# Optimization experiments

Hardware: AMD Instinct MI355X
Metric: run time of the kernel (lower is better)

The kernel has to match this reference:

```python
import jax, jax.numpy as jnp
import numpy as np

N_NODES = 100000
N_EDGES = 600000
HIDDEN = 128
BN_EPS = 1e-5


def setup_inputs() -> dict:
    key = jax.random.key(0)
    k_x, k_e, k_w, k_b, k_g = jax.random.split(key, 5)
    x = jax.random.normal(k_x, (N_NODES, HIDDEN), dtype=jnp.float32)
    edge_index = jax.random.randint(k_e, (2, N_EDGES), 0, N_NODES, dtype=jnp.int64)
    # GCNConv linear weight (no bias on the linear; bias added post-aggregation)
    scale = 1.0 / np.sqrt(HIDDEN)
    W = jax.random.uniform(k_w, (HIDDEN, HIDDEN), jnp.float32, -scale, scale)
    b = jax.random.uniform(k_b, (HIDDEN,), jnp.float32, -scale, scale)
    gamma = jnp.ones((HIDDEN,), jnp.float32)   # BatchNorm weight
    beta = jnp.zeros((HIDDEN,), jnp.float32)   # BatchNorm bias
    return {"x": x, "edge_index": edge_index, "W": W, "b": b, "gamma": gamma, "beta": beta}


def reference(x, edge_index, W, b, gamma, beta):
    N = x.shape[0]
    # ReLU then GCNConv linear transform: [N, D]
    h = jnp.matmul(jax.nn.relu(x), W)
    # Add self-loops (PyG GCNConv default)
    loops = jnp.arange(N, dtype=edge_index.dtype)
    row = jnp.concatenate([edge_index[0], loops])  # source nodes
    col = jnp.concatenate([edge_index[1], loops])  # target nodes
    # Symmetric normalization deg^{-1/2} with unit edge weights
    ones = jnp.ones(row.shape[0], dtype=h.dtype)
    deg = jax.ops.segment_sum(ones, col, num_segments=N)
    dinv = jnp.where(deg > 0, jax.lax.rsqrt(deg), 0.0)
    norm = dinv[row] * dinv[col]  # [E+N]
    # Gather -> scale -> scatter-add aggregation, then conv bias
    agg = jax.ops.segment_sum(norm[:, None] * h[row], col, num_segments=N)
    out = agg + b
    # BatchNorm1d (training mode: batch stats, biased variance)
    mean = jnp.mean(out, axis=0)
    var = jnp.var(out, axis=0)
    return gamma * (out - mean) * jax.lax.rsqrt(var + BN_EPS) + beta
```

## Files before the change

kernel.cpp:

```cpp
#include <hip/hip_runtime.h>

#define D 128
#define CAP 32
#define BN_EPS 1e-5f

typedef float floatx4 __attribute__((ext_vector_type(4)));
typedef __bf16 bf16x8 __attribute__((ext_vector_type(8)));

__device__ inline unsigned short f2bf(float f) {
    unsigned u; __builtin_memcpy(&u, &f, 4);
    unsigned r = (u + 0x7FFFu + ((u >> 16) & 1u)) >> 16;
    return (unsigned short)r;
}
__device__ inline float bflo(unsigned v) { unsigned x = v << 16; float f; __builtin_memcpy(&f, &x, 4); return f; }
__device__ inline float bfhi(unsigned v) { unsigned x = v & 0xFFFF0000u; float f; __builtin_memcpy(&f, &x, 4); return f; }

__global__ void setup_k(const unsigned* __restrict__ e, int* __restrict__ flag,
                        int* __restrict__ cursor, float* __restrict__ sums,
                        float* __restrict__ sumsq, const float* __restrict__ W,
                        unsigned short* __restrict__ Wt, int n_nodes) {
    int i = blockIdx.x * blockDim.x + threadIdx.x;
    if (i < n_nodes) cursor[i] = 0;
    if (i < D) { sums[i] = 0.f; sumsq[i] = 0.f; }
    if (i < D * D) {
        int n = i >> 7, k = i & 127;
        Wt[n * D + k] = f2bf(W[k * D + n]);
    }
    if (i == 0) {
        unsigned acc = 0;
        for (int k = 0; k < 64; ++k) acc |= e[2 * k + 1];
        *flag = (acc == 0u) ? 1 : 0;
    }
}

__global__ __launch_bounds__(256, 2) void gb_k(const float* __restrict__ x,
                                               const unsigned short* __restrict__ Wt,
                                               unsigned short* __restrict__ h,
                                               int n_mtiles, int gemm_blocks,
                                               const void* __restrict__ ep, const int* __restrict__ flag,
                                               int* __restrict__ cursor, int* __restrict__ bucket,
                                               int n_edges, int n_nodes) {
    if (blockIdx.x >= gemm_blocks) {
        int e = (blockIdx.x - gemm_blocks) * 256 + threadIdx.x;
        if (e >= n_edges) return;
        int r, c;
        if (*flag) {
            const long long* p = (const long long*)ep;
            r = (int)p[e]; c = (int)p[e + n_edges];
        } else {
            const int* p = (const int*)ep;
            r = p[e]; c = p[e + n_edges];
        }
        int pos = atomicAdd(&cursor[c], 1);
        if (pos < CAP) bucket[(size_t)pos * n_nodes + c] = r;
        return;
    }
    int lane = threadIdx.x & 63;
    int wave = blockIdx.x * 4 + (threadIdx.x >> 6);
    int nw = gemm_blocks * 4;
    int l15 = lane & 15;
    int quad = lane >> 4;

    bf16x8 Bf[4][8];
    for (int ks = 0; ks < 4; ++ks)
        for (int j = 0; j < 8; ++j)
            Bf[ks][j] = *(const bf16x8*)(Wt + (size_t)(j * 16 + l15) * D + ks * 32 + quad * 8);

    for (int mt = wave; mt < n_mtiles; mt += nw) {
        const float* xrow = x + (size_t)(mt * 16 + l15) * D + quad * 8;
        bf16x8 Af[4];
        for (int ks = 0; ks < 4; ++ks) {
            float4 a0 = *(const float4*)(xrow + ks * 32);
            float4 a1 = *(const float4*)(xrow + ks * 32 + 4);
            float av[8] = {a0.x, a0.y, a0.z, a0.w, a1.x, a1.y, a1.z, a1.w};
            union { unsigned short u[8]; bf16x8 v; } tmp;
            for (int jj = 0; jj < 8; ++jj) tmp.u[jj] = f2bf(fmaxf(av[jj], 0.0f));
            Af[ks] = tmp.v;
        }
        floatx4 acc[8];
        for (int j = 0; j < 8; ++j) acc[j] = (floatx4){0.f, 0.f, 0.f, 0.f};
        for (int ks = 0; ks < 4; ++ks)
            for (int j = 0; j < 8; ++j)
                acc[j] = __builtin_amdgcn_mfma_f32_16x16x32_bf16(Af[ks], Bf[ks][j], acc[j], 0, 0, 0);
        for (int j = 0; j < 8; ++j)
            for (int reg = 0; reg < 4; ++reg) {
                int rr = mt * 16 + quad * 4 + reg;
                int cc = j * 16 + l15;
                h[(size_t)rr * D + cc] = f2bf(acc[j][reg]);
            }
    }
}

__global__ void dinv_k(const int* __restrict__ cursor, float* __restrict__ dinv, int n_nodes) {
    int i = blockIdx.x * blockDim.x + threadIdx.x;
    if (i < n_nodes) dinv[i] = rsqrtf(1.0f + (float)cursor[i]);
}

#define SLOT(p) int rb##p = bucket[(p) * NN + node];                 \
                int r##p = ((p) < degc) ? rb##p : node;              \
                float w##p = ((p) < degc) ? dinv[r##p] : 0.0f;       \
                unsigned hv##p = hp[(unsigned)r##p * 64u + lane];
#define ACC(p)  { ax += w##p * bflo(hv##p); ay += w##p * bfhi(hv##p); }

__global__ __launch_bounds__(256) void agg_k(const unsigned short* __restrict__ h,
                                             const int* __restrict__ bucket,
                                             const int* __restrict__ cursor,
                                             const float* __restrict__ dinv,
                                             unsigned* __restrict__ aggb,
                                             int n_nodes) {
    int lane = threadIdx.x & 63;
    int node = __builtin_amdgcn_readfirstlane(blockIdx.x * 4 + (threadIdx.x >> 6));
    if (node >= n_nodes) return;
    const unsigned* hp = (const unsigned*)h;
    const int NN = n_nodes;

    int deg = cursor[node];
    int degc = deg < CAP ? deg : CAP;
    float dc = dinv[node];

    unsigned v = hp[(unsigned)node * 64u + lane];
    float ax = dc * bflo(v), ay = dc * bfhi(v);

    SLOT(0) SLOT(1) SLOT(2) SLOT(3) SLOT(4) SLOT(5) SLOT(6) SLOT(7)

    if (degc <= 8) {
        ACC(0) ACC(1) ACC(2) ACC(3) ACC(4) ACC(5) ACC(6) ACC(7)
    } else {
        SLOT(8) SLOT(9) SLOT(10) SLOT(11) SLOT(12) SLOT(13) SLOT(14) SLOT(15)
        ACC(0)  ACC(1)  ACC(2)  ACC(3)  ACC(4)  ACC(5)  ACC(6)  ACC(7)
        ACC(8)  ACC(9)  ACC(10) ACC(11) ACC(12) ACC(13) ACC(14) ACC(15)
        for (int p = 16; p < degc; ++p) {
            int r = bucket[p * NN + node];
            float w = dinv[r];
            unsigned hh = hp[(unsigned)r * 64u + lane];
            ax += w * bflo(hh); ay += w * bfhi(hh);
        }
    }

    float ox = dc * ax, oy = dc * ay;
    aggb[(unsigned)node * 64u + lane] = ((unsigned)f2bf(oy) << 16) | (unsigned)f2bf(ox);
}

__global__ __launch_bounds__(256) void stats_k(const unsigned* __restrict__ aggb,
                                               float* __restrict__ sums, float* __restrict__ sumsq,
                                               int n_nodes) {
    __shared__ float red[256];
    int lane = threadIdx.x & 63;
    int wib = threadIdx.x >> 6;
    int wave = blockIdx.x * 4 + wib;
    int nw = gridDim.x * 4;
    float s0 = 0.f, s1 = 0.f, q0 = 0.f, q1 = 0.f;
    int n = wave;
    for (; n + 3 * nw < n_nodes; n += 4 * nw) {
        unsigned p0 = aggb[(size_t)n * 64 + lane];
        unsigned p1 = aggb[(size_t)(n + nw) * 64 + lane];
        unsigned p2 = aggb[(size_t)(n + 2 * nw) * 64 + lane];
        unsigned p3 = aggb[(size_t)(n + 3 * nw) * 64 + lane];
        float a0 = bflo(p0), b0 = bfhi(p0), a1 = bflo(p1), b1 = bfhi(p1);
        float a2 = bflo(p2), b2 = bfhi(p2), a3 = bflo(p3), b3 = bfhi(p3);
        s0 += a0 + a1 + a2 + a3;
        s1 += b0 + b1 + b2 + b3;
        q0 += a0 * a0 + a1 * a1 + a2 * a2 + a3 * a3;
        q1 += b0 * b0 + b1 * b1 + b2 * b2 + b3 * b3;
    }
    for (; n < n_nodes; n += nw) {
        unsigned p = aggb[(size_t)n * 64 + lane];
        float vx = bflo(p), vy = bfhi(p);
        s0 += vx; s1 += vy; q0 += vx * vx; q1 += vy * vy;
    }
    red[threadIdx.x] = s0; __syncthreads();
    if (wib == 0) atomicAdd(&sums[2 * lane], red[lane] + red[64 + lane] + red[128 + lane] + red[192 + lane]);
    __syncthreads();
    red[threadIdx.x] = s1; __syncthreads();
    if (wib == 0) atomicAdd(&sums[2 * lane + 1], red[lane] + red[64 + lane] + red[128 + lane] + red[192 + lane]);
    __syncthreads();
    red[threadIdx.x] = q0; __syncthreads();
    if (wib == 0) atomicAdd(&sumsq[2 * lane], red[lane] + red[64 + lane] + red[128 + lane] + red[192 + lane]);
    __syncthreads();
    red[threadIdx.x] = q1; __syncthreads();
    if (wib == 0) atomicAdd(&sumsq[2 * lane + 1], red[lane] + red[64 + lane] + red[128 + lane] + red[192 + lane]);
}

__global__ __launch_bounds__(256) void final_k(const unsigned* __restrict__ aggb,
                                               const float* __restrict__ sums, const float* __restrict__ sumsq,
                                               const float* __restrict__ gamma, const float* __restrict__ beta,
                                               float* __restrict__ out, int total4, float inv_n) {
    int i = blockIdx.x * blockDim.x + threadIdx.x;
    if (i >= total4) return;
    int idx = i * 4;
    int f = idx & (D - 1);
    float4 sm = *(const float4*)(sums + f);
    float4 sq = *(const float4*)(sumsq + f);
    float4 g  = *(const float4*)(gamma + f);
    float4 bt = *(const float4*)(beta + f);
    uint2 p = *(const uint2*)(aggb + i * 2);

    float m0 = sm.x * inv_n, m1 = sm.y * inv_n, m2 = sm.z * inv_n, m3 = sm.w * inv_n;
    float sc0 = g.x * rsqrtf(sq.x * inv_n - m0 * m0 + BN_EPS);
    float sc1 = g.y * rsqrtf(sq.y * inv_n - m1 * m1 + BN_EPS);
    float sc2 = g.z * rsqrtf(sq.z * inv_n - m2 * m2 + BN_EPS);
    float sc3 = g.w * rsqrtf(sq.w * inv_n - m3 * m3 + BN_EPS);
    float4 o;
    o.x = fmaf(bflo(p.x), sc0, bt.x - m0 * sc0);
    o.y = fmaf(bfhi(p.x), sc1, bt.y - m1 * sc1);
    o.z = fmaf(bflo(p.y), sc2, bt.z - m2 * sc2);
    o.w = fmaf(bfhi(p.y), sc3, bt.w - m3 * sc3);
    *(float4*)(out + idx) = o;
}

extern "C" void kernel_launch(void* const* d_in, const int* in_sizes, int n_in,
                              void* d_out, int out_size, void* d_ws, size_t ws_size,
                              hipStream_t stream) {
    const float* x     = (const float*)d_in[0];
    const void*  edges = d_in[1];
    const float* W     = (const float*)d_in[2];
    const float* gamma = (const float*)d_in[4];
    const float* beta  = (const float*)d_in[5];
    float* out = (float*)d_out;

    int N = in_sizes[0] / D;
    int E = in_sizes[1] / 2;

    char* ws = (char*)d_ws;
    size_t off = 0;
    auto alloc = [&](size_t bytes) { void* p = ws + off; off += (bytes + 255) & ~(size_t)255; return p; };
    unsigned short* h  = (unsigned short*)alloc((size_t)N * D * 2);
    unsigned* aggb     = (unsigned*)alloc((size_t)N * D * 2);
    int* bucket        = (int*)alloc((size_t)N * CAP * 4);
    int* cursor        = (int*)alloc((size_t)N * 4);
    float* dinv        = (float*)alloc((size_t)N * 4);
    unsigned short* Wt = (unsigned short*)alloc((size_t)D * D * 2);
    float* sums        = (float*)alloc(512);
    float* sumsq       = (float*)alloc(512);
    int* flag          = (int*)alloc(16);

    int nblk = (N + 255) / 256;
    int n_mtiles = N / 16;
    int gemm_blocks = (n_mtiles + 3) / 4;
    int bucket_blocks = (E + 255) / 256;

    setup_k<<<nblk, 256, 0, stream>>>((const unsigned*)edges, flag, cursor, sums, sumsq, W, Wt, N);
    gb_k<<<gemm_blocks + bucket_blocks, 256, 0, stream>>>(x, Wt, h, n_mtiles, gemm_blocks,
                                                          edges, flag, cursor, bucket, E, N);
    dinv_k<<<nblk, 256, 0, stream>>>(cursor, dinv, N);
    agg_k<<<(N + 3) / 4, 256, 0, stream>>>(h, bucket, cursor, dinv, aggb, N);
    stats_k<<<512, 256, 0, stream>>>(aggb, sums, sumsq, N);
    final_k<<<(N * D / 4 + 255) / 256, 256, 0, stream>>>(aggb, sums, sumsq, gamma, beta, out, N * D / 4, 1.0f / (float)N);
}
```

Before: 272.6 us.

## Interleave GEMM and bucket blocks, node-major buckets, inline dinv computation

Gemm and edge-bucketing blocks are now spread evenly across the grid instead of all GEMM blocks coming first, so the two kinds of work run at the same time. The bucket array becomes node-major, so each node's neighbour list is contiguous for the aggregation reads. The separate dinv kernel is removed and rsqrt of degree is computed inline from cursor inside aggregation. Launch bounds occupancy for gb_k rises from 2 to 4 blocks, and the stats grid grows to 2048 blocks. The catch is that scatter writes in bucketing become scattered across rows, and aggregation recomputes rsqrt per neighbour.

```diff
diff --git a/kernel.cpp b/kernel.cpp
--- a/kernel.cpp
+++ b/kernel.cpp
@@ -33,15 +33,18 @@
     }
 }
 
-__global__ __launch_bounds__(256, 2) void gb_k(const float* __restrict__ x,
+__global__ __launch_bounds__(256, 4) void gb_k(const float* __restrict__ x,
                                                const unsigned short* __restrict__ Wt,
                                                unsigned short* __restrict__ h,
-                                               int n_mtiles, int gemm_blocks,
+                                               int n_mtiles, int gemm_blocks, int total_blocks,
                                                const void* __restrict__ ep, const int* __restrict__ flag,
                                                int* __restrict__ cursor, int* __restrict__ bucket,
-                                               int n_edges, int n_nodes) {
-    if (blockIdx.x >= gemm_blocks) {
-        int e = (blockIdx.x - gemm_blocks) * 256 + threadIdx.x;
+                                               int n_edges) {
+    int b = blockIdx.x;
+    int gi = (int)((long long)b * gemm_blocks / total_blocks);
+    int gi1 = (int)(((long long)b + 1) * gemm_blocks / total_blocks);
+    if (gi1 == gi) {
+        int e = (b - gi) * 256 + threadIdx.x;
         if (e >= n_edges) return;
         int r, c;
         if (*flag) {
@@ -52,11 +55,11 @@
             r = p[e]; c = p[e + n_edges];
         }
         int pos = atomicAdd(&cursor[c], 1);
-        if (pos < CAP) bucket[(size_t)pos * n_nodes + c] = r;
+        if (pos < CAP) bucket[(size_t)c * CAP + pos] = r;
         return;
     }
     int lane = threadIdx.x & 63;
-    int wave = blockIdx.x * 4 + (threadIdx.x >> 6);
+    int wave = gi * 4 + (threadIdx.x >> 6);
     int nw = gemm_blocks * 4;
     int l15 = lane & 15;
     int quad = lane >> 4;
@@ -91,35 +94,29 @@
     }
 }
 
-__global__ void dinv_k(const int* __restrict__ cursor, float* __restrict__ dinv, int n_nodes) {
-    int i = blockIdx.x * blockDim.x + threadIdx.x;
-    if (i < n_nodes) dinv[i] = rsqrtf(1.0f + (float)cursor[i]);
-}
-
-#define SLOT(p) int rb##p = bucket[(p) * NN + node];                 \
-                int r##p = ((p) < degc) ? rb##p : node;              \
-                float w##p = ((p) < degc) ? dinv[r##p] : 0.0f;       \
+#define SLOT(p) int rb##p = bk[p];                                        \
+                int r##p = ((p) < degc) ? rb##p : node;                   \
+                float w##p = ((p) < degc) ? rsqrtf(1.0f + (float)cursor[r##p]) : 0.0f; \
                 unsigned hv##p = hp[(unsigned)r##p * 64u + lane];
 #define ACC(p)  { ax += w##p * bflo(hv##p); ay += w##p * bfhi(hv##p); }
 
 __global__ __launch_bounds__(256) void agg_k(const unsigned short* __restrict__ h,
                                              const int* __restrict__ bucket,
                                              const int* __restrict__ cursor,
-                                             const float* __restrict__ dinv,
                                              unsigned* __restrict__ aggb,
                                              int n_nodes) {
     int lane = threadIdx.x & 63;
     int node = __builtin_amdgcn_readfirstlane(blockIdx.x * 4 + (threadIdx.x >> 6));
     if (node >= n_nodes) return;
     const unsigned* hp = (const unsigned*)h;
-    const int NN = n_nodes;
 
     int deg = cursor[node];
     int degc = deg < CAP ? deg : CAP;
-    float dc = dinv[node];
+    float dc = rsqrtf(1.0f + (float)deg);
 
     unsigned v = hp[(unsigned)node * 64u + lane];
     float ax = dc * bflo(v), ay = dc * bfhi(v);
+    const int* bk = bucket + (size_t)node * CAP;
 
     SLOT(0) SLOT(1) SLOT(2) SLOT(3) SLOT(4) SLOT(5) SLOT(6) SLOT(7)
 
@@ -130,8 +127,8 @@
         ACC(0)  ACC(1)  ACC(2)  ACC(3)  ACC(4)  ACC(5)  ACC(6)  ACC(7)
         ACC(8)  ACC(9)  ACC(10) ACC(11) ACC(12) ACC(13) ACC(14) ACC(15)
         for (int p = 16; p < degc; ++p) {
-            int r = bucket[p * NN + node];
-            float w = dinv[r];
+            int r = bk[p];
+            float w = rsqrtf(1.0f + (float)cursor[r]);
             unsigned hh = hp[(unsigned)r * 64u + lane];
             ax += w * bflo(hh); ay += w * bfhi(hh);
         }
@@ -228,7 +225,6 @@
     unsigned* aggb     = (unsigned*)alloc((size_t)N * D * 2);
     int* bucket        = (int*)alloc((size_t)N * CAP * 4);
     int* cursor        = (int*)alloc((size_t)N * 4);
-    float* dinv        = (float*)alloc((size_t)N * 4);
     unsigned short* Wt = (unsigned short*)alloc((size_t)D * D * 2);
     float* sums        = (float*)alloc(512);
     float* sumsq       = (float*)alloc(512);
@@ -238,12 +234,12 @@
     int n_mtiles = N / 16;
     int gemm_blocks = (n_mtiles + 3) / 4;
     int bucket_blocks = (E + 255) / 256;
+    int total_blocks = gemm_blocks + bucket_blocks;
 
     setup_k<<<nblk, 256, 0, stream>>>((const unsigned*)edges, flag, cursor, sums, sumsq, W, Wt, N);
-    gb_k<<<gemm_blocks + bucket_blocks, 256, 0, stream>>>(x, Wt, h, n_mtiles, gemm_blocks,
-                                                          edges, flag, cursor, bucket, E, N);
-    dinv_k<<<nblk, 256, 0, stream>>>(cursor, dinv, N);
-    agg_k<<<(N + 3) / 4, 256, 0, stream>>>(h, bucket, cursor, dinv, aggb, N);
-    stats_k<<<512, 256, 0, stream>>>(aggb, sums, sumsq, N);
+    gb_k<<<total_blocks, 256, 0, stream>>>(x, Wt, h, n_mtiles, gemm_blocks, total_blocks,
+                                           edges, flag, cursor, bucket, E);
+    agg_k<<<(N + 3) / 4, 256, 0, stream>>>(h, bucket, cursor, aggb, N);
+    stats_k<<<2048, 256, 0, stream>>>(aggb, sums, sumsq, N);
     final_k<<<(N * D / 4 + 255) / 256, 256, 0, stream>>>(aggb, sums, sumsq, gamma, beta, out, N * D / 4, 1.0f / (float)N);
 }
```

Result: slower. 375.8 us (+37.9%).
